# Optimization experiments

Hardware: AMD Instinct MI355X
Metric: run time of the kernel (lower is better)

## Reference

```python
import jax, jax.numpy as jnp
import numpy as np

N, D_IN, UNITS = 8192, 4096, 4096

def setup_inputs() -> dict:
    key = jax.random.key(0)
    k1, k2 = jax.random.split(key)
    x = jax.random.normal(k1, (N, D_IN), dtype=jnp.float32)
    # weight initialized RandomNormal(stddev=0.1) in the original build()
    w = jax.random.normal(k2, (D_IN, UNITS), dtype=jnp.float32) * 0.1
    return {"x": x, "w": w}

def reference(x, w):
    # BinaryDense: sign-binarize both activations and weights, then dense matmul.
    # tf.sign semantics: sign(0) == 0, matched by jnp.sign.
    x_bin = jnp.sign(x)  # [N, d_in]
    w_bin = jnp.sign(w)  # [d_in, units]
    return jnp.matmul(x_bin, w_bin)  # [N, units]
```

## Files before the change

### kernel.cpp

```cpp
#include <hip/hip_runtime.h>
#include <stdint.h>

#define M_DIM 8192
#define K_DIM 4096
#define N_DIM 4096
#define KB (K_DIM / 2)

typedef unsigned char u8;
typedef unsigned int u32;
typedef int i32x4 __attribute__((ext_vector_type(4)));
typedef int i32x8 __attribute__((ext_vector_type(8)));
typedef float f32x4 __attribute__((ext_vector_type(4)));
typedef float float4v __attribute__((ext_vector_type(4)));
typedef u32 u32x2 __attribute__((ext_vector_type(2)));

__device__ __forceinline__ u32 sign_fp4(float v) {
  return v > 0.0f ? 0x2u : (v < 0.0f ? 0xAu : 0x0u);
}

__global__ void binarize_fused(const float* __restrict__ x, const float* __restrict__ w,
                               u32* __restrict__ xb, u8* __restrict__ wT) {
  const int tid = threadIdx.x;
  if (blockIdx.x < 4096) {
    __shared__ u8 tile[64][65];
    const int bid = blockIdx.x;
    const int bn = (bid & 63) * 64;
    const int bk = (bid >> 6) * 64;

#pragma unroll
    for (int it = 0; it < 4; ++it) {
      int idx = tid + it * 256;
      int r = idx >> 4;
      int c = (idx & 15) * 4;
      float4v v = *(const float4v*)&w[(size_t)(bk + r) * N_DIM + bn + c];
      tile[c + 0][r] = (u8)sign_fp4(v.x);
      tile[c + 1][r] = (u8)sign_fp4(v.y);
      tile[c + 2][r] = (u8)sign_fp4(v.z);
      tile[c + 3][r] = (u8)sign_fp4(v.w);
    }
    __syncthreads();
    const int rn = tid >> 2;
    const int cb = (tid & 3) * 8;
    u32x2 o;
    u32 lo = 0, hi = 0;
#pragma unroll
    for (int j = 0; j < 4; ++j) {
      lo |= (u32)(tile[rn][cb * 2 + 2 * j] | (tile[rn][cb * 2 + 2 * j + 1] << 4)) << (8 * j);
      hi |= (u32)(tile[rn][cb * 2 + 8 + 2 * j] | (tile[rn][cb * 2 + 9 + 2 * j] << 4)) << (8 * j);
    }
    o.x = lo;
    o.y = hi;
    *(u32x2*)&wT[(size_t)(bn + rn) * KB + (bk >> 1) + cb] = o;
  } else {
    const int n8 = M_DIM * K_DIM / 8;
    int i = (blockIdx.x - 4096) * 256 + tid;
    const int stride = 2048 * 256;
    for (; i < n8; i += stride) {
      float4v v0 = ((const float4v*)x)[2 * i];
      float4v v1 = ((const float4v*)x)[2 * i + 1];
      u32 wd = sign_fp4(v0.x) | (sign_fp4(v0.y) << 4) | (sign_fp4(v0.z) << 8) |
               (sign_fp4(v0.w) << 12) | (sign_fp4(v1.x) << 16) | (sign_fp4(v1.y) << 20) |
               (sign_fp4(v1.z) << 24) | (sign_fp4(v1.w) << 28);
      xb[i] = wd;
    }
  }
}

#define BM 256
#define BN 256
#define BKB 128
#define NT (K_DIM / 256)

__device__ __forceinline__ void gload_lds16(const u8* g, u8* l) {
  __builtin_amdgcn_global_load_lds(
      (const __attribute__((address_space(1))) void*)g,
      (__attribute__((address_space(3))) void*)l, 16, 0, 0);
}

__device__ __forceinline__ i32x8 pad8(i32x4 v) {
  return __builtin_shufflevector(v, v, 0, 1, 2, 3, -1, -1, -1, -1);
}

__device__ __forceinline__ f32x4 mfma_fp4(i32x4 a, i32x4 b, f32x4 c) {
  return __builtin_amdgcn_mfma_scale_f32_16x16x128_f8f6f4(pad8(a), pad8(b), c, 4, 4, 0, 0x7F, 0,
                                                          0x7F);
}

__global__ __launch_bounds__(512, 2) void gemm_bin_fp4(const u8* __restrict__ A,
                                                       const u8* __restrict__ Bt,
                                                       float* __restrict__ C) {
  __shared__ u8 lds[2][4][128 * 128];

  const int tid = threadIdx.x;
  const int lane = tid & 63;
  const int wid = tid >> 6;
  const int wr = wid >> 2;
  const int wc = wid & 3;

  const int b = blockIdx.x;
  const int sw = (b & 7) * (gridDim.x >> 3) + (b >> 3);
  const int tiles_n = N_DIM / BN;
  const int bm = (sw / tiles_n) * BM;
  const int bn = (sw % tiles_n) * BN;

  const int l15 = lane & 15;
  const int g4 = lane >> 4;
  const int srow = lane >> 3;
  const int swz_src = (((lane & 7) ^ srow) << 4);

  auto stage = [&](int buf, int slot, const u8* gbase) {
#pragma unroll
    for (int i = 0; i < 2; ++i) {
      const u8* g = gbase + (size_t)(i * 64 + wid * 8 + srow) * KB + swz_src;
      gload_lds16(g, &lds[buf][slot][(i * 64 + wid * 8) * 128]);
    }
  };

  f32x4 acc[8][4] = {};

  {
    const u8* Abase = A + (size_t)bm * KB;
    const u8* Bbase = Bt + (size_t)bn * KB;
    stage(0, 0, Abase);
    stage(0, 1, Abase + (size_t)128 * KB);
    stage(0, 2, Bbase);
    stage(0, 3, Bbase + (size_t)128 * KB);
    stage(1, 2, Bbase + BKB);
    stage(1, 3, Bbase + (size_t)128 * KB + BKB);
  }
  asm volatile("s_waitcnt vmcnt(4)" ::: "memory");
  __builtin_amdgcn_s_barrier();

  i32x4 a[4][2], b01[2][2], b23[2][2];

  for (int t = 0; t < NT; ++t) {
    const int buf = t & 1;
    const u8* As = &lds[buf][wr][0];
    const u8* Bs = &lds[buf][2 + (wc >> 1)][0];
    const int brow0 = (wc & 1) * 64;
    const u8* Anext = A + (size_t)bm * KB + (t + 1) * BKB;
    const u8* Bnext2 = Bt + (size_t)bn * KB + (t + 2) * BKB;

#pragma unroll
    for (int m = 0; m < 4; ++m)
#pragma unroll
      for (int kk = 0; kk < 2; ++kk) {
        int row = m * 16 + l15;
        int col = (kk * 64 + g4 * 16) ^ ((row & 7) << 4);
        a[m][kk] = *(const i32x4*)&As[row * 128 + col];
      }
#pragma unroll
    for (int n = 0; n < 2; ++n)
#pragma unroll
      for (int kk = 0; kk < 2; ++kk) {
        int row = brow0 + n * 16 + l15;
        int col = (kk * 64 + g4 * 16) ^ ((row & 7) << 4);
        b01[n][kk] = *(const i32x4*)&Bs[row * 128 + col];
      }
    if (t + 1 < NT) stage(buf ^ 1, 0, Anext);
    __builtin_amdgcn_s_barrier();
    asm volatile("s_waitcnt lgkmcnt(0)" ::: "memory");
    __builtin_amdgcn_sched_barrier(0);
    __builtin_amdgcn_s_setprio(1);
#pragma unroll
    for (int kk = 0; kk < 2; ++kk)
#pragma unroll
      for (int m = 0; m < 4; ++m)
#pragma unroll
        for (int n = 0; n < 2; ++n)
          acc[m][n] = mfma_fp4(a[m][kk], b01[n][kk], acc[m][n]);
    __builtin_amdgcn_s_setprio(0);
    __builtin_amdgcn_s_barrier();

#pragma unroll
    for (int n = 0; n < 2; ++n)
#pragma unroll
      for (int kk = 0; kk < 2; ++kk) {
        int row = brow0 + (2 + n) * 16 + l15;
        int col = (kk * 64 + g4 * 16) ^ ((row & 7) << 4);
        b23[n][kk] = *(const i32x4*)&Bs[row * 128 + col];
      }
    if (t + 1 < NT) stage(buf ^ 1, 1, Anext + (size_t)128 * KB);
    __builtin_amdgcn_s_barrier();
    asm volatile("s_waitcnt lgkmcnt(0)" ::: "memory");
    __builtin_amdgcn_sched_barrier(0);
    __builtin_amdgcn_s_setprio(1);
#pragma unroll
    for (int kk = 0; kk < 2; ++kk)
#pragma unroll
      for (int m = 0; m < 4; ++m)
#pragma unroll
        for (int n = 0; n < 2; ++n)
          acc[m][2 + n] = mfma_fp4(a[m][kk], b23[n][kk], acc[m][2 + n]);
    __builtin_amdgcn_s_setprio(0);
    __builtin_amdgcn_s_barrier();

#pragma unroll
    for (int m = 0; m < 4; ++m)
#pragma unroll
      for (int kk = 0; kk < 2; ++kk) {
        int row = 64 + m * 16 + l15;
        int col = (kk * 64 + g4 * 16) ^ ((row & 7) << 4);
        a[m][kk] = *(const i32x4*)&As[row * 128 + col];
      }
    if (t + 2 < NT) stage(buf, 2, Bnext2);
    __builtin_amdgcn_s_barrier();
    asm volatile("s_waitcnt lgkmcnt(0)" ::: "memory");
    __builtin_amdgcn_sched_barrier(0);
    __builtin_amdgcn_s_setprio(1);
#pragma unroll
    for (int kk = 0; kk < 2; ++kk)
#pragma unroll
      for (int m = 0; m < 4; ++m)
#pragma unroll
        for (int n = 0; n < 2; ++n)
          acc[4 + m][n] = mfma_fp4(a[m][kk], b01[n][kk], acc[4 + m][n]);
    __builtin_amdgcn_s_setprio(0);
    __builtin_amdgcn_s_barrier();

    if (t + 2 < NT) stage(buf, 3, Bnext2 + (size_t)128 * KB);
    __builtin_amdgcn_s_barrier();
    __builtin_amdgcn_s_setprio(1);
#pragma unroll
    for (int kk = 0; kk < 2; ++kk)
#pragma unroll
      for (int m = 0; m < 4; ++m)
#pragma unroll
        for (int n = 0; n < 2; ++n)
          acc[4 + m][2 + n] = mfma_fp4(a[m][kk], b23[n][kk], acc[4 + m][2 + n]);
    __builtin_amdgcn_s_setprio(0);
    if (t + 2 < NT)
      asm volatile("s_waitcnt vmcnt(4)" ::: "memory");
    else
      asm volatile("s_waitcnt vmcnt(0)" ::: "memory");
    __builtin_amdgcn_s_barrier();
  }

  const int crow0 = bm + wr * 128;
  const int ccol0 = bn + wc * 64;
#pragma unroll
  for (int m = 0; m < 8; ++m)
#pragma unroll
    for (int n = 0; n < 4; ++n)
#pragma unroll
      for (int j = 0; j < 4; ++j)
        C[(size_t)(crow0 + m * 16 + g4 * 4 + j) * N_DIM + ccol0 + n * 16 + l15] = acc[m][n][j];
}

__global__ void naive_bin_gemm(const float* __restrict__ X, const float* __restrict__ W,
                               float* __restrict__ C) {
  int j = blockIdx.x * blockDim.x + threadIdx.x;
  int i = blockIdx.y;
  if (j >= N_DIM) return;
  float s = 0.0f;
  for (int k = 0; k < K_DIM; ++k) {
    float xv = X[(size_t)i * K_DIM + k];
    float wv = W[(size_t)k * N_DIM + j];
    float sx = (float)((xv > 0.0f) - (xv < 0.0f));
    float sw = (float)((wv > 0.0f) - (wv < 0.0f));
    s += sx * sw;
  }
  C[(size_t)i * N_DIM + j] = s;
}

extern "C" void kernel_launch(void* const* d_in, const int* in_sizes, int n_in,
                              void* d_out, int out_size, void* d_ws, size_t ws_size,
                              hipStream_t stream) {
  const float* x = (const float*)d_in[0];
  const float* w = (const float*)d_in[1];
  float* out = (float*)d_out;

  const size_t xb_bytes = (size_t)M_DIM * KB;
  const size_t wt_bytes = (size_t)N_DIM * KB;

  if (ws_size >= xb_bytes + wt_bytes) {
    u8* xb = (u8*)d_ws;
    u8* wt = (u8*)((char*)d_ws + xb_bytes);

    binarize_fused<<<4096 + 2048, 256, 0, stream>>>(x, w, (u32*)xb, wt);

    const int grid = (M_DIM / BM) * (N_DIM / BN);
    gemm_bin_fp4<<<grid, 512, 0, stream>>>(xb, wt, out);
  } else {
    naive_bin_gemm<<<dim3(N_DIM / 256, M_DIM), dim3(256), 0, stream>>>(x, w, out);
  }
}
```

Before: 127.9 us.

## Reorder MFMA K-split phases and vectorize weight nibble packing via word loads

The main GEMM loop is reorganized so each of the four phases covers one K-half (kk) over all four N sub-tiles, instead of one N-half over both K-halves. This keeps fewer A fragments live (av[4] instead of a[4][2]) and holds two B sets split by K, which changes register pressure and the LDS-read-to-MFMA interleave. An extra lgkmcnt wait is added before the last phase because A is now reloaded there. The weight binarize kernel pads its tile rows to 68 bytes and packs nibbles from 32-bit LDS word reads with shift/mask instead of per-byte reads.

```diff
diff --git a/kernel.cpp b/kernel.cpp
--- a/kernel.cpp
+++ b/kernel.cpp
@@ -18,11 +18,15 @@
   return v > 0.0f ? 0x2u : (v < 0.0f ? 0xAu : 0x0u);
 }
 
+__device__ __forceinline__ u32 pk16(u32 v) {
+  return (v & 0xFu) | ((v >> 4) & 0xF0u) | ((v >> 8) & 0xF00u) | ((v >> 12) & 0xF000u);
+}
+
 __global__ void binarize_fused(const float* __restrict__ x, const float* __restrict__ w,
                                u32* __restrict__ xb, u8* __restrict__ wT) {
   const int tid = threadIdx.x;
   if (blockIdx.x < 4096) {
-    __shared__ u8 tile[64][65];
+    __shared__ u8 tile[64][68];
     const int bid = blockIdx.x;
     const int bn = (bid & 63) * 64;
     const int bk = (bid >> 6) * 64;
@@ -40,17 +44,16 @@
     }
     __syncthreads();
     const int rn = tid >> 2;
-    const int cb = (tid & 3) * 8;
+    const int cbyte = (tid & 3) * 8;
+    const u32* trow = (const u32*)&tile[rn][0];
+    u32 q0 = trow[cbyte / 2 + 0];
+    u32 q1 = trow[cbyte / 2 + 1];
+    u32 q2 = trow[cbyte / 2 + 2];
+    u32 q3 = trow[cbyte / 2 + 3];
     u32x2 o;
-    u32 lo = 0, hi = 0;
-#pragma unroll
-    for (int j = 0; j < 4; ++j) {
-      lo |= (u32)(tile[rn][cb * 2 + 2 * j] | (tile[rn][cb * 2 + 2 * j + 1] << 4)) << (8 * j);
-      hi |= (u32)(tile[rn][cb * 2 + 8 + 2 * j] | (tile[rn][cb * 2 + 9 + 2 * j] << 4)) << (8 * j);
-    }
-    o.x = lo;
-    o.y = hi;
-    *(u32x2*)&wT[(size_t)(bn + rn) * KB + (bk >> 1) + cb] = o;
+    o.x = pk16(q0) | (pk16(q1) << 16);
+    o.y = pk16(q2) | (pk16(q3) << 16);
+    *(u32x2*)&wT[(size_t)(bn + rn) * KB + (bk >> 1) + cbyte] = o;
   } else {
     const int n8 = M_DIM * K_DIM / 8;
     int i = (blockIdx.x - 4096) * 256 + tid;
@@ -131,7 +134,7 @@
   asm volatile("s_waitcnt vmcnt(4)" ::: "memory");
   __builtin_amdgcn_s_barrier();
 
-  i32x4 a[4][2], b01[2][2], b23[2][2];
+  i32x4 av[4], b0[4], b1[4];
 
   for (int t = 0; t < NT; ++t) {
     const int buf = t & 1;
@@ -142,92 +145,90 @@
     const u8* Bnext2 = Bt + (size_t)bn * KB + (t + 2) * BKB;
 
 #pragma unroll
-    for (int m = 0; m < 4; ++m)
-#pragma unroll
-      for (int kk = 0; kk < 2; ++kk) {
-        int row = m * 16 + l15;
-        int col = (kk * 64 + g4 * 16) ^ ((row & 7) << 4);
-        a[m][kk] = *(const i32x4*)&As[row * 128 + col];
-      }
-#pragma unroll
-    for (int n = 0; n < 2; ++n)
-#pragma unroll
-      for (int kk = 0; kk < 2; ++kk) {
-        int row = brow0 + n * 16 + l15;
-        int col = (kk * 64 + g4 * 16) ^ ((row & 7) << 4);
-        b01[n][kk] = *(const i32x4*)&Bs[row * 128 + col];
-      }
+    for (int m = 0; m < 4; ++m) {
+      int row = m * 16 + l15;
+      int col = (g4 * 16) ^ ((row & 7) << 4);
+      av[m] = *(const i32x4*)&As[row * 128 + col];
+    }
+#pragma unroll
+    for (int n = 0; n < 4; ++n) {
+      int row = brow0 + n * 16 + l15;
+      int col = (g4 * 16) ^ ((row & 7) << 4);
+      b0[n] = *(const i32x4*)&Bs[row * 128 + col];
+    }
     if (t + 1 < NT) stage(buf ^ 1, 0, Anext);
     __builtin_amdgcn_s_barrier();
     asm volatile("s_waitcnt lgkmcnt(0)" ::: "memory");
     __builtin_amdgcn_sched_barrier(0);
     __builtin_amdgcn_s_setprio(1);
 #pragma unroll
-    for (int kk = 0; kk < 2; ++kk)
-#pragma unroll
-      for (int m = 0; m < 4; ++m)
-#pragma unroll
-        for (int n = 0; n < 2; ++n)
-          acc[m][n] = mfma_fp4(a[m][kk], b01[n][kk], acc[m][n]);
-    __builtin_amdgcn_s_setprio(0);
-    __builtin_amdgcn_s_barrier();
-
-#pragma unroll
-    for (int n = 0; n < 2; ++n)
-#pragma unroll
-      for (int kk = 0; kk < 2; ++kk) {
-        int row = brow0 + (2 + n) * 16 + l15;
-        int col = (kk * 64 + g4 * 16) ^ ((row & 7) << 4);
-        b23[n][kk] = *(const i32x4*)&Bs[row * 128 + col];
-      }
+    for (int m = 0; m < 4; ++m)
+#pragma unroll
+      for (int n = 0; n < 4; ++n)
+        acc[m][n] = mfma_fp4(av[m], b0[n], acc[m][n]);
+    __builtin_amdgcn_s_setprio(0);
+    __builtin_amdgcn_s_barrier();
+
+#pragma unroll
+    for (int m = 0; m < 4; ++m) {
+      int row = m * 16 + l15;
+      int col = (64 + g4 * 16) ^ ((row & 7) << 4);
+      av[m] = *(const i32x4*)&As[row * 128 + col];
+    }
+#pragma unroll
+    for (int n = 0; n < 4; ++n) {
+      int row = brow0 + n * 16 + l15;
+      int col = (64 + g4 * 16) ^ ((row & 7) << 4);
+      b1[n] = *(const i32x4*)&Bs[row * 128 + col];
+    }
     if (t + 1 < NT) stage(buf ^ 1, 1, Anext + (size_t)128 * KB);
     __builtin_amdgcn_s_barrier();
     asm volatile("s_waitcnt lgkmcnt(0)" ::: "memory");
     __builtin_amdgcn_sched_barrier(0);
     __builtin_amdgcn_s_setprio(1);
 #pragma unroll
-    for (int kk = 0; kk < 2; ++kk)
-#pragma unroll
-      for (int m = 0; m < 4; ++m)
-#pragma unroll
-        for (int n = 0; n < 2; ++n)
-          acc[m][2 + n] = mfma_fp4(a[m][kk], b23[n][kk], acc[m][2 + n]);
-    __builtin_amdgcn_s_setprio(0);
-    __builtin_amdgcn_s_barrier();
-
-#pragma unroll
-    for (int m = 0; m < 4; ++m)
-#pragma unroll
-      for (int kk = 0; kk < 2; ++kk) {
-        int row = 64 + m * 16 + l15;
-        int col = (kk * 64 + g4 * 16) ^ ((row & 7) << 4);
-        a[m][kk] = *(const i32x4*)&As[row * 128 + col];
-      }
+    for (int m = 0; m < 4; ++m)
+#pragma unroll
+      for (int n = 0; n < 4; ++n)
+        acc[m][n] = mfma_fp4(av[m], b1[n], acc[m][n]);
+    __builtin_amdgcn_s_setprio(0);
+    __builtin_amdgcn_s_barrier();
+
+#pragma unroll
+    for (int m = 0; m < 4; ++m) {
+      int row = 64 + m * 16 + l15;
+      int col = (g4 * 16) ^ ((row & 7) << 4);
+      av[m] = *(const i32x4*)&As[row * 128 + col];
+    }
     if (t + 2 < NT) stage(buf, 2, Bnext2);
     __builtin_amdgcn_s_barrier();
     asm volatile("s_waitcnt lgkmcnt(0)" ::: "memory");
     __builtin_amdgcn_sched_barrier(0);
     __builtin_amdgcn_s_setprio(1);
 #pragma unroll
-    for (int kk = 0; kk < 2; ++kk)
-#pragma unroll
-      for (int m = 0; m < 4; ++m)
-#pragma unroll
-        for (int n = 0; n < 2; ++n)
-          acc[4 + m][n] = mfma_fp4(a[m][kk], b01[n][kk], acc[4 + m][n]);
-    __builtin_amdgcn_s_setprio(0);
-    __builtin_amdgcn_s_barrier();
-
+    for (int m = 0; m < 4; ++m)
+#pragma unroll
+      for (int n = 0; n < 4; ++n)
+        acc[4 + m][n] = mfma_fp4(av[m], b0[n], acc[4 + m][n]);
+    __builtin_amdgcn_s_setprio(0);
+    __builtin_amdgcn_s_barrier();
+
+#pragma unroll
+    for (int m = 0; m < 4; ++m) {
+      int row = 64 + m * 16 + l15;
+      int col = (64 + g4 * 16) ^ ((row & 7) << 4);
+      av[m] = *(const i32x4*)&As[row * 128 + col];
+    }
     if (t + 2 < NT) stage(buf, 3, Bnext2 + (size_t)128 * KB);
     __builtin_amdgcn_s_barrier();
-    __builtin_amdgcn_s_setprio(1);
-#pragma unroll
-    for (int kk = 0; kk < 2; ++kk)
-#pragma unroll
-      for (int m = 0; m < 4; ++m)
-#pragma unroll
-        for (int n = 0; n < 2; ++n)
-          acc[4 + m][2 + n] = mfma_fp4(a[m][kk], b23[n][kk], acc[4 + m][2 + n]);
+    asm volatile("s_waitcnt lgkmcnt(0)" ::: "memory");
+    __builtin_amdgcn_sched_barrier(0);
+    __builtin_amdgcn_s_setprio(1);
+#pragma unroll
+    for (int m = 0; m < 4; ++m)
+#pragma unroll
+      for (int n = 0; n < 4; ++n)
+        acc[4 + m][n] = mfma_fp4(av[m], b1[n], acc[4 + m][n]);
     __builtin_amdgcn_s_setprio(0);
     if (t + 2 < NT)
       asm volatile("s_waitcnt vmcnt(4)" ::: "memory");
```

After: 127.4 us. Within noise of the previous version (-0.4%).
